# Optimization experiments

Measured on AMD Instinct MI355X. Metric: run time of the kernel, lower is better.

Reference implementation:

```python
import jax, jax.numpy as jnp
import numpy as np

B, S, D = 1, 8192, 4096
D_OUT = 4096
FP_FEATURES = 256
BITS = 4
MAXQ = float(2 ** BITS - 1)  # 15.0


def setup_inputs() -> dict:
    key = jax.random.key(0)
    kx, kw, kb, ks = jax.random.split(key, 4)
    x = jax.random.normal(kx, (B, S, D), dtype=jnp.float32)
    weight = jax.random.normal(kw, (D_OUT, D), dtype=jnp.float32) * 0.02
    bias = jax.random.normal(kb, (D_OUT,), dtype=jnp.float32) * 0.02
    # act_scales -> sorted indices; top FP_FEATURES stay in fp, rest quantized
    act_scales = jax.random.uniform(ks, (D,), dtype=jnp.float32)
    order = jnp.argsort(act_scales)
    q_idx = order[:-FP_FEATURES].astype(jnp.int64)
    fp_idx = order[-FP_FEATURES:].astype(jnp.int64)
    return {"x": x, "weight": weight, "bias": bias, "q_idx": q_idx, "fp_idx": fp_idx}


def reference(x, weight, bias, q_idx, fp_idx):
    # gather features to be quantized: [B, S, Dq]
    qf = x[:, :, q_idx]
    # per-token asymmetric quant params (find_params)
    xmin = jnp.minimum(qf.min(axis=-1), 0.0)
    xmax = jnp.maximum(qf.max(axis=-1), 0.0)
    both_zero = (xmin == 0.0) & (xmax == 0.0)
    xmin = jnp.where(both_zero, -1.0, xmin)
    xmax = jnp.where(both_zero, 1.0, xmax)
    scale = ((xmax - xmin) / MAXQ)[..., None]   # [B, S, 1]
    zero = jnp.round(-xmin[..., None] / scale)  # [B, S, 1]
    # asymmetric_quantize (fake quant)
    q = jnp.clip(jnp.round(qf / scale) + zero, 0.0, MAXQ)
    qf = scale * (q - zero)
    # scatter quantized + fp features back into a zeros_like buffer
    mixed = jnp.zeros_like(x)
    mixed = mixed.at[:, :, q_idx].set(qf)
    mixed = mixed.at[:, :, fp_idx].set(x[:, :, fp_idx])
    # wrapped Linear
    return mixed @ weight.T + bias
```

## Files before the change

### kernel.cpp

```cpp
#include <hip/hip_runtime.h>


typedef __attribute__((ext_vector_type(8))) short short8;
typedef __attribute__((ext_vector_type(4))) float f32x4;
typedef __attribute__((ext_vector_type(4))) int int4v;

#define S_ROWS 8192
#define D_IN   4096
#define D_OUTC 4096
#define MAXQF  15.0f

__device__ __forceinline__ unsigned short f2bf(float f) {
  unsigned int u = __float_as_uint(f);
  u += 0x7FFFu + ((u >> 16) & 1u);
  return (unsigned short)(u >> 16);
}

__global__ __launch_bounds__(256) void prep_kernel(const float* __restrict__ x,
                                                   const float* __restrict__ W,
                                                   const int* __restrict__ fp_idx,
                                                   signed char* __restrict__ actq,
                                                   signed char* __restrict__ wq,
                                                   short* __restrict__ xfp,
                                                   short* __restrict__ wfp,
                                                   float* __restrict__ as_,
                                                   float* __restrict__ ws_) {
  const int bid = blockIdx.x;
  const int t = threadIdx.x;
  __shared__ float s_r[4];

  if (bid >= S_ROWS) {
    const int row = bid - S_ROWS;
    const float* wr = W + (size_t)row * D_IN;
    float4 v[4];
    float mx = 0.0f;
#pragma unroll
    for (int i = 0; i < 4; ++i) {
      v[i] = ((const float4*)wr)[i * 256 + t];
      mx = fmaxf(mx, fmaxf(fmaxf(fabsf(v[i].x), fabsf(v[i].y)),
                           fmaxf(fabsf(v[i].z), fabsf(v[i].w))));
    }
#pragma unroll
    for (int d = 32; d > 0; d >>= 1) mx = fmaxf(mx, __shfl_xor(mx, d));
    if ((t & 63) == 0) s_r[t >> 6] = mx;
    __syncthreads();
    mx = fmaxf(fmaxf(s_r[0], s_r[1]), fmaxf(s_r[2], s_r[3]));
    const float wsr = (mx > 0.0f) ? (mx / 127.0f) : 1.0f;

    unsigned int* wrow = (unsigned int*)(wq + (size_t)row * D_IN);
#pragma unroll
    for (int i = 0; i < 4; ++i) {
      const float in[4] = { v[i].x, v[i].y, v[i].z, v[i].w };
      unsigned int pk = 0;
#pragma unroll
      for (int j = 0; j < 4; ++j) {
        int q = (int)fminf(fmaxf(rintf(in[j] / wsr), -127.0f), 127.0f);
        pk |= ((unsigned int)(unsigned char)(signed char)q) << (8 * j);
      }
      wrow[i * 256 + t] = pk;
    }
    wfp[(size_t)row * 256 + t] = (short)f2bf(wr[fp_idx[t]]);
    if (t == 0) ws_[row] = wsr;
    return;
  }

  __shared__ unsigned char fl[4096];
  ((int4*)fl)[t] = make_int4(0, 0, 0, 0);
  __syncthreads();
  fl[fp_idx[t]] = 1;
  __syncthreads();

  const int row = bid;
  const float* xr = x + (size_t)row * D_IN;

  float4 v[4];
  unsigned int fw[4];
  float mn = 0.0f, mx = 0.0f;
#pragma unroll
  for (int i = 0; i < 4; ++i) {
    const int idx = i * 256 + t;
    v[i] = ((const float4*)xr)[idx];
    fw[i] = ((const unsigned int*)fl)[idx];
    if (!(fw[i] & 0x000000FFu)) { mn = fminf(mn, v[i].x); mx = fmaxf(mx, v[i].x); }
    if (!(fw[i] & 0x0000FF00u)) { mn = fminf(mn, v[i].y); mx = fmaxf(mx, v[i].y); }
    if (!(fw[i] & 0x00FF0000u)) { mn = fminf(mn, v[i].z); mx = fmaxf(mx, v[i].z); }
    if (!(fw[i] & 0xFF000000u)) { mn = fminf(mn, v[i].w); mx = fmaxf(mx, v[i].w); }
  }
  __shared__ float s_mn[4];
#pragma unroll
  for (int d = 32; d > 0; d >>= 1) {
    mn = fminf(mn, __shfl_xor(mn, d));
    mx = fmaxf(mx, __shfl_xor(mx, d));
  }
  if ((t & 63) == 0) { s_mn[t >> 6] = mn; s_r[t >> 6] = mx; }
  __syncthreads();
  mn = fminf(fminf(s_mn[0], s_mn[1]), fminf(s_mn[2], s_mn[3]));
  mx = fmaxf(fmaxf(s_r[0], s_r[1]), fmaxf(s_r[2], s_r[3]));
  if (mn == 0.0f && mx == 0.0f) { mn = -1.0f; mx = 1.0f; }
  const float scale = (mx - mn) / MAXQF;
  const float zp = rintf(-mn / scale);
  const int zpi = (int)zp;

  unsigned int* arow = (unsigned int*)(actq + (size_t)row * D_IN);
#pragma unroll
  for (int i = 0; i < 4; ++i) {
    const int idx = i * 256 + t;
    const float in[4] = { v[i].x, v[i].y, v[i].z, v[i].w };
    const unsigned int f = fw[i];
    unsigned int pk = 0;
#pragma unroll
    for (int j = 0; j < 4; ++j) {
      int q = (int)fminf(fmaxf(rintf(in[j] / scale) + zp, 0.0f), MAXQF) - zpi;
      if ((f >> (8 * j)) & 0xFFu) q = 0;
      pk |= ((unsigned int)(unsigned char)(signed char)q) << (8 * j);
    }
    arow[idx] = pk;
  }
  xfp[(size_t)row * 256 + t] = (short)f2bf(xr[fp_idx[t]]);
  if (t == 0) as_[row] = scale;
}


__device__ __forceinline__ void gl2lds16(const void* g, const void* l) {
  __builtin_amdgcn_global_load_lds(
      (const __attribute__((address_space(1))) unsigned int*)g,
      (__attribute__((address_space(3))) unsigned int*)l, 16, 0, 0);
}

#define BARRIER()  asm volatile("s_barrier" ::: "memory")
#define LGKM0()    asm volatile("s_waitcnt lgkmcnt(0)" ::: "memory")

__global__ __launch_bounds__(512) void gemm_fp_kernel(const short* __restrict__ A,
                                                      const short* __restrict__ Bw,
                                                      const float* __restrict__ bias,
                                                      float* __restrict__ C) {
  __shared__ __align__(16) short lds[65536];
  const int tid = threadIdx.x;
  const int l   = tid & 63;
  const int w   = tid >> 6;
  const int wr  = w >> 2;
  const int wc  = w & 3;
  const int bid = blockIdx.x;
  const int swz = (bid & 7) * 64 + (bid >> 3);
  const int bm  = swz >> 4;
  const int bn  = swz & 15;

  const int c16  = ((l & 7) ^ (l >> 3)) * 8;
  const int rib0 = (w * 2 + 0) * 8 + (l >> 3);
  const int rib1 = (w * 2 + 1) * 8 + (l >> 3);
  const int d0   = (w * 2 + 0) * 512;
  const int d1   = (w * 2 + 1) * 512;
  const int LDK  = 256;

  const short* bA00 = A  + (size_t)(bm * 256 +   0 + rib0) * LDK + c16;
  const short* bA01 = A  + (size_t)(bm * 256 +   0 + rib1) * LDK + c16;
  const short* bA10 = A  + (size_t)(bm * 256 + 128 + rib0) * LDK + c16;
  const short* bA11 = A  + (size_t)(bm * 256 + 128 + rib1) * LDK + c16;
  const short* bB00 = Bw + (size_t)(bn * 256 +   0 + rib0) * LDK + c16;
  const short* bB01 = Bw + (size_t)(bn * 256 +   0 + rib1) * LDK + c16;
  const short* bB10 = Bw + (size_t)(bn * 256 + 128 + rib0) * LDK + c16;
  const short* bB11 = Bw + (size_t)(bn * 256 + 128 + rib1) * LDK + c16;

  gl2lds16(bA00, &lds[0 + d0]);          gl2lds16(bA01, &lds[0 + d1]);
  gl2lds16(bA10, &lds[8192 + d0]);       gl2lds16(bA11, &lds[8192 + d1]);
  gl2lds16(bB00, &lds[16384 + d0]);      gl2lds16(bB01, &lds[16384 + d1]);
  gl2lds16(bB10, &lds[24576 + d0]);      gl2lds16(bB11, &lds[24576 + d1]);
  gl2lds16(bA00 + 64, &lds[32768 + d0]); gl2lds16(bA01 + 64, &lds[32768 + d1]);
  gl2lds16(bA10 + 64, &lds[40960 + d0]); gl2lds16(bA11 + 64, &lds[40960 + d1]);
  asm volatile("s_waitcnt vmcnt(4)" ::: "memory");
  BARRIER();

  const short* pA00 = bA00 + 128; const short* pA01 = bA01 + 128;
  const short* pA10 = bA10 + 128; const short* pA11 = bA11 + 128;
  const short* pB00 = bB00 + 64;  const short* pB01 = bB01 + 64;
  const short* pB10 = bB10 + 64;  const short* pB11 = bB11 + 64;

  const int ch0  = ((l >> 4) ^ (l & 7)) * 8;
  const int aoff = wr * 8192 + (l & 15) * 64;
  const int boff = 16384 + (wc >> 1) * 8192 + (wc & 1) * 4096 + (l & 15) * 64;

  f32x4 acc[8][4] = {};
  int bo = 0;

  for (int t = 0; t < 4; ++t) {
    const int nxt = bo ^ 32768;
    short8 a0[4][2], a1[4][2], b[2][2];

#pragma unroll
    for (int m = 0; m < 4; ++m) {
      a0[m][0] = *(const short8*)&lds[bo + aoff + m * 1024 + ch0];
      a0[m][1] = *(const short8*)&lds[bo + aoff + m * 1024 + (ch0 ^ 32)];
    }
#pragma unroll
    for (int n = 0; n < 2; ++n) {
      b[n][0] = *(const short8*)&lds[bo + boff + n * 1024 + ch0];
      b[n][1] = *(const short8*)&lds[bo + boff + n * 1024 + (ch0 ^ 32)];
    }
    if (t < 3) { gl2lds16(pB00, &lds[nxt + 16384 + d0]);
                 gl2lds16(pB01, &lds[nxt + 16384 + d1]); }
    asm volatile("s_waitcnt lgkmcnt(8)" ::: "memory");
    BARRIER();
    LGKM0();
    __builtin_amdgcn_s_setprio(1);
#pragma unroll
    for (int m = 0; m < 4; ++m)
#pragma unroll
      for (int n = 0; n < 2; ++n) {
        acc[m][n] = __builtin_amdgcn_mfma_f32_16x16x32_bf16(a0[m][0], b[n][0], acc[m][n], 0, 0, 0);
        acc[m][n] = __builtin_amdgcn_mfma_f32_16x16x32_bf16(a0[m][1], b[n][1], acc[m][n], 0, 0, 0);
      }
    __builtin_amdgcn_s_setprio(0);
    BARRIER();

#pragma unroll
    for (int m = 0; m < 4; ++m) {
      a1[m][0] = *(const short8*)&lds[bo + aoff + (m + 4) * 1024 + ch0];
      a1[m][1] = *(const short8*)&lds[bo + aoff + (m + 4) * 1024 + (ch0 ^ 32)];
    }
    if (t < 3) { gl2lds16(pB10, &lds[nxt + 24576 + d0]);
                 gl2lds16(pB11, &lds[nxt + 24576 + d1]); }
    BARRIER();
    LGKM0();
    __builtin_amdgcn_s_setprio(1);
#pragma unroll
    for (int m = 0; m < 4; ++m)
#pragma unroll
      for (int n = 0; n < 2; ++n) {
        acc[m + 4][n] = __builtin_amdgcn_mfma_f32_16x16x32_bf16(a1[m][0], b[n][0], acc[m + 4][n], 0, 0, 0);
        acc[m + 4][n] = __builtin_amdgcn_mfma_f32_16x16x32_bf16(a1[m][1], b[n][1], acc[m + 4][n], 0, 0, 0);
      }
    __builtin_amdgcn_s_setprio(0);
    BARRIER();

#pragma unroll
    for (int n = 0; n < 2; ++n) {
      b[n][0] = *(const short8*)&lds[bo + boff + (n + 2) * 1024 + ch0];
      b[n][1] = *(const short8*)&lds[bo + boff + (n + 2) * 1024 + (ch0 ^ 32)];
    }
    if (t < 2) { gl2lds16(pA00, &lds[bo + 0 + d0]);
                 gl2lds16(pA01, &lds[bo + 0 + d1]); }
    BARRIER();
    LGKM0();
    __builtin_amdgcn_s_setprio(1);
#pragma unroll
    for (int m = 0; m < 4; ++m)
#pragma unroll
      for (int n = 0; n < 2; ++n) {
        acc[m + 4][n + 2] = __builtin_amdgcn_mfma_f32_16x16x32_bf16(a1[m][0], b[n][0], acc[m + 4][n + 2], 0, 0, 0);
        acc[m + 4][n + 2] = __builtin_amdgcn_mfma_f32_16x16x32_bf16(a1[m][1], b[n][1], acc[m + 4][n + 2], 0, 0, 0);
      }
    __builtin_amdgcn_s_setprio(0);
    BARRIER();

    if (t < 2) { gl2lds16(pA10, &lds[bo + 8192 + d0]);
                 gl2lds16(pA11, &lds[bo + 8192 + d1]); }
    BARRIER();
    __builtin_amdgcn_s_setprio(1);
#pragma unroll
    for (int m = 0; m < 4; ++m)
#pragma unroll
      for (int n = 0; n < 2; ++n) {
        acc[m][n + 2] = __builtin_amdgcn_mfma_f32_16x16x32_bf16(a0[m][0], b[n][0], acc[m][n + 2], 0, 0, 0);
        acc[m][n + 2] = __builtin_amdgcn_mfma_f32_16x16x32_bf16(a0[m][1], b[n][1], acc[m][n + 2], 0, 0, 0);
      }
    __builtin_amdgcn_s_setprio(0);
    if (t < 2) { asm volatile("s_waitcnt vmcnt(4)" ::: "memory"); }
    else       { asm volatile("s_waitcnt vmcnt(0)" ::: "memory"); }
    BARRIER();

    pA00 += 64; pA01 += 64; pA10 += 64; pA11 += 64;
    pB00 += 64; pB01 += 64; pB10 += 64; pB11 += 64;
    bo = nxt;
  }

  const int row0 = bm * 256 + wr * 128 + ((l >> 4) << 2);
  const int col0 = bn * 256 + wc * 64 + (l & 15);
#pragma unroll
  for (int m = 0; m < 8; ++m)
#pragma unroll
    for (int n = 0; n < 4; ++n) {
      const int col = col0 + n * 16;
      const float bv = bias[col];
#pragma unroll
      for (int r = 0; r < 4; ++r)
        C[(size_t)(row0 + m * 16 + r) * D_OUTC + col] = acc[m][n][r] + bv;
    }
}

__global__ __launch_bounds__(512) void gemm_i8_kernel(const signed char* __restrict__ A,
                                                      const signed char* __restrict__ Bw,
                                                      const float* __restrict__ as_,
                                                      const float* __restrict__ ws_,
                                                      float* __restrict__ C) {
  __shared__ __align__(16) signed char lds[131072];
  const int tid = threadIdx.x;
  const int l   = tid & 63;
  const int w   = tid >> 6;
  const int wr  = w >> 2;
  const int wc  = w & 3;
  const int bid = blockIdx.x;
  const int swz = (bid & 7) * 64 + (bid >> 3);
  const int bm  = swz >> 4;
  const int bn  = swz & 15;

  const int c16  = ((l & 7) ^ (l >> 3)) * 16;
  const int rib0 = (w * 2 + 0) * 8 + (l >> 3);
  const int rib1 = (w * 2 + 1) * 8 + (l >> 3);
  const int d0   = (w * 2 + 0) * 1024;
  const int d1   = (w * 2 + 1) * 1024;

  const signed char* bA00 = A  + (size_t)(bm * 256 +   0 + rib0) * D_IN + c16;
  const signed char* bA01 = A  + (size_t)(bm * 256 +   0 + rib1) * D_IN + c16;
  const signed char* bA10 = A  + (size_t)(bm * 256 + 128 + rib0) * D_IN + c16;
  const signed char* bA11 = A  + (size_t)(bm * 256 + 128 + rib1) * D_IN + c16;
  const signed char* bB00 = Bw + (size_t)(bn * 256 +   0 + rib0) * D_IN + c16;
  const signed char* bB01 = Bw + (size_t)(bn * 256 +   0 + rib1) * D_IN + c16;
  const signed char* bB10 = Bw + (size_t)(bn * 256 + 128 + rib0) * D_IN + c16;
  const signed char* bB11 = Bw + (size_t)(bn * 256 + 128 + rib1) * D_IN + c16;

  gl2lds16(bA00, &lds[0 + d0]);           gl2lds16(bA01, &lds[0 + d1]);
  gl2lds16(bA10, &lds[16384 + d0]);       gl2lds16(bA11, &lds[16384 + d1]);
  gl2lds16(bB00, &lds[32768 + d0]);       gl2lds16(bB01, &lds[32768 + d1]);
  gl2lds16(bB10, &lds[49152 + d0]);       gl2lds16(bB11, &lds[49152 + d1]);
  gl2lds16(bA00 + 128, &lds[65536 + d0]); gl2lds16(bA01 + 128, &lds[65536 + d1]);
  gl2lds16(bA10 + 128, &lds[81920 + d0]); gl2lds16(bA11 + 128, &lds[81920 + d1]);
  asm volatile("s_waitcnt vmcnt(4)" ::: "memory");
  BARRIER();

  const signed char* pA00 = bA00 + 256; const signed char* pA01 = bA01 + 256;
  const signed char* pA10 = bA10 + 256; const signed char* pA11 = bA11 + 256;
  const signed char* pB00 = bB00 + 128; const signed char* pB01 = bB01 + 128;
  const signed char* pB10 = bB10 + 128; const signed char* pB11 = bB11 + 128;

  const int ch0  = ((l >> 4) ^ (l & 7)) * 16;
  const int aoff = wr * 16384 + (l & 15) * 128;
  const int boff = 32768 + (wc >> 1) * 16384 + (wc & 1) * 8192 + (l & 15) * 128;

  int4v acc[8][4] = {};
  int bo = 0;

  for (int t = 0; t < 32; ++t) {
    const int nxt = bo ^ 65536;
    int4v a0[4][2], a1[4][2], b[2][2];

#pragma unroll
    for (int m = 0; m < 4; ++m) {
      a0[m][0] = *(const int4v*)&lds[bo + aoff + m * 2048 + ch0];
      a0[m][1] = *(const int4v*)&lds[bo + aoff + m * 2048 + (ch0 ^ 64)];
    }
#pragma unroll
    for (int n = 0; n < 2; ++n) {
      b[n][0] = *(const int4v*)&lds[bo + boff + n * 2048 + ch0];
      b[n][1] = *(const int4v*)&lds[bo + boff + n * 2048 + (ch0 ^ 64)];
    }
    if (t < 31) { gl2lds16(pB00, &lds[nxt + 32768 + d0]);
                  gl2lds16(pB01, &lds[nxt + 32768 + d1]); }
    asm volatile("s_waitcnt lgkmcnt(8)" ::: "memory");
    BARRIER();
    LGKM0();
    __builtin_amdgcn_s_setprio(1);
#pragma unroll
    for (int m = 0; m < 4; ++m)
#pragma unroll
      for (int n = 0; n < 2; ++n) {
        acc[m][n] = __builtin_amdgcn_mfma_i32_16x16x64_i8(a0[m][0], b[n][0], acc[m][n], 0, 0, 0);
        acc[m][n] = __builtin_amdgcn_mfma_i32_16x16x64_i8(a0[m][1], b[n][1], acc[m][n], 0, 0, 0);
      }
    __builtin_amdgcn_s_setprio(0);
    BARRIER();

#pragma unroll
    for (int m = 0; m < 4; ++m) {
      a1[m][0] = *(const int4v*)&lds[bo + aoff + (m + 4) * 2048 + ch0];
      a1[m][1] = *(const int4v*)&lds[bo + aoff + (m + 4) * 2048 + (ch0 ^ 64)];
    }
    if (t < 31) { gl2lds16(pB10, &lds[nxt + 49152 + d0]);
                  gl2lds16(pB11, &lds[nxt + 49152 + d1]); }
    BARRIER();
    LGKM0();
    __builtin_amdgcn_s_setprio(1);
#pragma unroll
    for (int m = 0; m < 4; ++m)
#pragma unroll
      for (int n = 0; n < 2; ++n) {
        acc[m + 4][n] = __builtin_amdgcn_mfma_i32_16x16x64_i8(a1[m][0], b[n][0], acc[m + 4][n], 0, 0, 0);
        acc[m + 4][n] = __builtin_amdgcn_mfma_i32_16x16x64_i8(a1[m][1], b[n][1], acc[m + 4][n], 0, 0, 0);
      }
    __builtin_amdgcn_s_setprio(0);
    BARRIER();

#pragma unroll
    for (int n = 0; n < 2; ++n) {
      b[n][0] = *(const int4v*)&lds[bo + boff + (n + 2) * 2048 + ch0];
      b[n][1] = *(const int4v*)&lds[bo + boff + (n + 2) * 2048 + (ch0 ^ 64)];
    }
    if (t < 30) { gl2lds16(pA00, &lds[bo + 0 + d0]);
                  gl2lds16(pA01, &lds[bo + 0 + d1]); }
    BARRIER();
    LGKM0();
    __builtin_amdgcn_s_setprio(1);
#pragma unroll
    for (int m = 0; m < 4; ++m)
#pragma unroll
      for (int n = 0; n < 2; ++n) {
        acc[m + 4][n + 2] = __builtin_amdgcn_mfma_i32_16x16x64_i8(a1[m][0], b[n][0], acc[m + 4][n + 2], 0, 0, 0);
        acc[m + 4][n + 2] = __builtin_amdgcn_mfma_i32_16x16x64_i8(a1[m][1], b[n][1], acc[m + 4][n + 2], 0, 0, 0);
      }
    __builtin_amdgcn_s_setprio(0);
    BARRIER();

    if (t < 30) { gl2lds16(pA10, &lds[bo + 16384 + d0]);
                  gl2lds16(pA11, &lds[bo + 16384 + d1]); }
    BARRIER();
    __builtin_amdgcn_s_setprio(1);
#pragma unroll
    for (int m = 0; m < 4; ++m)
#pragma unroll
      for (int n = 0; n < 2; ++n) {
        acc[m][n + 2] = __builtin_amdgcn_mfma_i32_16x16x64_i8(a0[m][0], b[n][0], acc[m][n + 2], 0, 0, 0);
        acc[m][n + 2] = __builtin_amdgcn_mfma_i32_16x16x64_i8(a0[m][1], b[n][1], acc[m][n + 2], 0, 0, 0);
      }
    __builtin_amdgcn_s_setprio(0);
    if (t < 30) { asm volatile("s_waitcnt vmcnt(4)" ::: "memory"); }
    else        { asm volatile("s_waitcnt vmcnt(0)" ::: "memory"); }
    BARRIER();

    pA00 += 128; pA01 += 128; pA10 += 128; pA11 += 128;
    pB00 += 128; pB01 += 128; pB10 += 128; pB11 += 128;
    bo = nxt;
  }

  const int row0 = bm * 256 + wr * 128 + ((l >> 4) << 2);
  const int col0 = bn * 256 + wc * 64 + (l & 15);
#pragma unroll
  for (int m = 0; m < 8; ++m)
#pragma unroll
    for (int n = 0; n < 4; ++n) {
      const int col = col0 + n * 16;
      const float wsv = ws_[col];
#pragma unroll
      for (int r = 0; r < 4; ++r) {
        const int row = row0 + m * 16 + r;
        const float s = as_[row] * wsv;
        float* cp = &C[(size_t)row * D_OUTC + col];
        *cp = *cp + s * (float)acc[m][n][r];
      }
    }
}

extern "C" void kernel_launch(void* const* d_in, const int* in_sizes, int n_in,
                              void* d_out, int out_size, void* d_ws, size_t ws_size,
                              hipStream_t stream) {
  const float* x    = (const float*)d_in[0];
  const float* W    = (const float*)d_in[1];
  const float* bias = (const float*)d_in[2];
  const int* fp_idx = (const int*)d_in[4];

  char* ws = (char*)d_ws;
  signed char* actq = (signed char*)ws;
  signed char* wq   = (signed char*)(ws + (32u << 20));
  short* xfp        = (short*)(ws + (48u << 20));
  short* wfp        = (short*)(ws + (52u << 20));
  float* as_        = (float*)(ws + (54u << 20));
  float* ws_        = (float*)(ws + (54u << 20) + (64u << 10));
  float* out = (float*)d_out;

  prep_kernel<<<S_ROWS + D_OUTC, 256, 0, stream>>>(x, W, fp_idx, actq, wq,
                                                   xfp, wfp, as_, ws_);
  gemm_fp_kernel<<<512, 512, 0, stream>>>(xfp, wfp, bias, out);
  gemm_i8_kernel<<<512, 512, 0, stream>>>(actq, wq, as_, ws_, out);
}
```

Measured before the change: 251.1 us.

## Fuse fp16 outlier GEMM into int8 GEMM kernel epilogue

Merges the separate bf16 outlier GEMM and int8 GEMM into one kernel. After the int8 main loop, accumulators are dequantized into float registers, then the bf16 K=256 GEMM accumulates on top, reusing the same LDS buffer, and bias is added on the single store. This removes one full write and read-modify-write pass over the fp32 output and one kernel launch, at the cost of a longer kernel and possible register pressure from the added launch bound.

```diff
diff --git a/kernel.cpp b/kernel.cpp
--- a/kernel.cpp
+++ b/kernel.cpp
@@ -130,168 +130,11 @@
 #define BARRIER()  asm volatile("s_barrier" ::: "memory")
 #define LGKM0()    asm volatile("s_waitcnt lgkmcnt(0)" ::: "memory")
 
-__global__ __launch_bounds__(512) void gemm_fp_kernel(const short* __restrict__ A,
-                                                      const short* __restrict__ Bw,
-                                                      const float* __restrict__ bias,
-                                                      float* __restrict__ C) {
-  __shared__ __align__(16) short lds[65536];
-  const int tid = threadIdx.x;
-  const int l   = tid & 63;
-  const int w   = tid >> 6;
-  const int wr  = w >> 2;
-  const int wc  = w & 3;
-  const int bid = blockIdx.x;
-  const int swz = (bid & 7) * 64 + (bid >> 3);
-  const int bm  = swz >> 4;
-  const int bn  = swz & 15;
-
-  const int c16  = ((l & 7) ^ (l >> 3)) * 8;
-  const int rib0 = (w * 2 + 0) * 8 + (l >> 3);
-  const int rib1 = (w * 2 + 1) * 8 + (l >> 3);
-  const int d0   = (w * 2 + 0) * 512;
-  const int d1   = (w * 2 + 1) * 512;
-  const int LDK  = 256;
-
-  const short* bA00 = A  + (size_t)(bm * 256 +   0 + rib0) * LDK + c16;
-  const short* bA01 = A  + (size_t)(bm * 256 +   0 + rib1) * LDK + c16;
-  const short* bA10 = A  + (size_t)(bm * 256 + 128 + rib0) * LDK + c16;
-  const short* bA11 = A  + (size_t)(bm * 256 + 128 + rib1) * LDK + c16;
-  const short* bB00 = Bw + (size_t)(bn * 256 +   0 + rib0) * LDK + c16;
-  const short* bB01 = Bw + (size_t)(bn * 256 +   0 + rib1) * LDK + c16;
-  const short* bB10 = Bw + (size_t)(bn * 256 + 128 + rib0) * LDK + c16;
-  const short* bB11 = Bw + (size_t)(bn * 256 + 128 + rib1) * LDK + c16;
-
-  gl2lds16(bA00, &lds[0 + d0]);          gl2lds16(bA01, &lds[0 + d1]);
-  gl2lds16(bA10, &lds[8192 + d0]);       gl2lds16(bA11, &lds[8192 + d1]);
-  gl2lds16(bB00, &lds[16384 + d0]);      gl2lds16(bB01, &lds[16384 + d1]);
-  gl2lds16(bB10, &lds[24576 + d0]);      gl2lds16(bB11, &lds[24576 + d1]);
-  gl2lds16(bA00 + 64, &lds[32768 + d0]); gl2lds16(bA01 + 64, &lds[32768 + d1]);
-  gl2lds16(bA10 + 64, &lds[40960 + d0]); gl2lds16(bA11 + 64, &lds[40960 + d1]);
-  asm volatile("s_waitcnt vmcnt(4)" ::: "memory");
-  BARRIER();
-
-  const short* pA00 = bA00 + 128; const short* pA01 = bA01 + 128;
-  const short* pA10 = bA10 + 128; const short* pA11 = bA11 + 128;
-  const short* pB00 = bB00 + 64;  const short* pB01 = bB01 + 64;
-  const short* pB10 = bB10 + 64;  const short* pB11 = bB11 + 64;
-
-  const int ch0  = ((l >> 4) ^ (l & 7)) * 8;
-  const int aoff = wr * 8192 + (l & 15) * 64;
-  const int boff = 16384 + (wc >> 1) * 8192 + (wc & 1) * 4096 + (l & 15) * 64;
-
-  f32x4 acc[8][4] = {};
-  int bo = 0;
-
-  for (int t = 0; t < 4; ++t) {
-    const int nxt = bo ^ 32768;
-    short8 a0[4][2], a1[4][2], b[2][2];
-
-#pragma unroll
-    for (int m = 0; m < 4; ++m) {
-      a0[m][0] = *(const short8*)&lds[bo + aoff + m * 1024 + ch0];
-      a0[m][1] = *(const short8*)&lds[bo + aoff + m * 1024 + (ch0 ^ 32)];
-    }
-#pragma unroll
-    for (int n = 0; n < 2; ++n) {
-      b[n][0] = *(const short8*)&lds[bo + boff + n * 1024 + ch0];
-      b[n][1] = *(const short8*)&lds[bo + boff + n * 1024 + (ch0 ^ 32)];
-    }
-    if (t < 3) { gl2lds16(pB00, &lds[nxt + 16384 + d0]);
-                 gl2lds16(pB01, &lds[nxt + 16384 + d1]); }
-    asm volatile("s_waitcnt lgkmcnt(8)" ::: "memory");
-    BARRIER();
-    LGKM0();
-    __builtin_amdgcn_s_setprio(1);
-#pragma unroll
-    for (int m = 0; m < 4; ++m)
-#pragma unroll
-      for (int n = 0; n < 2; ++n) {
-        acc[m][n] = __builtin_amdgcn_mfma_f32_16x16x32_bf16(a0[m][0], b[n][0], acc[m][n], 0, 0, 0);
-        acc[m][n] = __builtin_amdgcn_mfma_f32_16x16x32_bf16(a0[m][1], b[n][1], acc[m][n], 0, 0, 0);
-      }
-    __builtin_amdgcn_s_setprio(0);
-    BARRIER();
-
-#pragma unroll
-    for (int m = 0; m < 4; ++m) {
-      a1[m][0] = *(const short8*)&lds[bo + aoff + (m + 4) * 1024 + ch0];
-      a1[m][1] = *(const short8*)&lds[bo + aoff + (m + 4) * 1024 + (ch0 ^ 32)];
-    }
-    if (t < 3) { gl2lds16(pB10, &lds[nxt + 24576 + d0]);
-                 gl2lds16(pB11, &lds[nxt + 24576 + d1]); }
-    BARRIER();
-    LGKM0();
-    __builtin_amdgcn_s_setprio(1);
-#pragma unroll
-    for (int m = 0; m < 4; ++m)
-#pragma unroll
-      for (int n = 0; n < 2; ++n) {
-        acc[m + 4][n] = __builtin_amdgcn_mfma_f32_16x16x32_bf16(a1[m][0], b[n][0], acc[m + 4][n], 0, 0, 0);
-        acc[m + 4][n] = __builtin_amdgcn_mfma_f32_16x16x32_bf16(a1[m][1], b[n][1], acc[m + 4][n], 0, 0, 0);
-      }
-    __builtin_amdgcn_s_setprio(0);
-    BARRIER();
-
-#pragma unroll
-    for (int n = 0; n < 2; ++n) {
-      b[n][0] = *(const short8*)&lds[bo + boff + (n + 2) * 1024 + ch0];
-      b[n][1] = *(const short8*)&lds[bo + boff + (n + 2) * 1024 + (ch0 ^ 32)];
-    }
-    if (t < 2) { gl2lds16(pA00, &lds[bo + 0 + d0]);
-                 gl2lds16(pA01, &lds[bo + 0 + d1]); }
-    BARRIER();
-    LGKM0();
-    __builtin_amdgcn_s_setprio(1);
-#pragma unroll
-    for (int m = 0; m < 4; ++m)
-#pragma unroll
-      for (int n = 0; n < 2; ++n) {
-        acc[m + 4][n + 2] = __builtin_amdgcn_mfma_f32_16x16x32_bf16(a1[m][0], b[n][0], acc[m + 4][n + 2], 0, 0, 0);
-        acc[m + 4][n + 2] = __builtin_amdgcn_mfma_f32_16x16x32_bf16(a1[m][1], b[n][1], acc[m + 4][n + 2], 0, 0, 0);
-      }
-    __builtin_amdgcn_s_setprio(0);
-    BARRIER();
-
-    if (t < 2) { gl2lds16(pA10, &lds[bo + 8192 + d0]);
-                 gl2lds16(pA11, &lds[bo + 8192 + d1]); }
-    BARRIER();
-    __builtin_amdgcn_s_setprio(1);
-#pragma unroll
-    for (int m = 0; m < 4; ++m)
-#pragma unroll
-      for (int n = 0; n < 2; ++n) {
-        acc[m][n + 2] = __builtin_amdgcn_mfma_f32_16x16x32_bf16(a0[m][0], b[n][0], acc[m][n + 2], 0, 0, 0);
-        acc[m][n + 2] = __builtin_amdgcn_mfma_f32_16x16x32_bf16(a0[m][1], b[n][1], acc[m][n + 2], 0, 0, 0);
-      }
-    __builtin_amdgcn_s_setprio(0);
-    if (t < 2) { asm volatile("s_waitcnt vmcnt(4)" ::: "memory"); }
-    else       { asm volatile("s_waitcnt vmcnt(0)" ::: "memory"); }
-    BARRIER();
-
-    pA00 += 64; pA01 += 64; pA10 += 64; pA11 += 64;
-    pB00 += 64; pB01 += 64; pB10 += 64; pB11 += 64;
-    bo = nxt;
-  }
-
-  const int row0 = bm * 256 + wr * 128 + ((l >> 4) << 2);
-  const int col0 = bn * 256 + wc * 64 + (l & 15);
-#pragma unroll
-  for (int m = 0; m < 8; ++m)
-#pragma unroll
-    for (int n = 0; n < 4; ++n) {
-      const int col = col0 + n * 16;
-      const float bv = bias[col];
-#pragma unroll
-      for (int r = 0; r < 4; ++r)
-        C[(size_t)(row0 + m * 16 + r) * D_OUTC + col] = acc[m][n][r] + bv;
-    }
-}
-
-__global__ __launch_bounds__(512) void gemm_i8_kernel(const signed char* __restrict__ A,
-                                                      const signed char* __restrict__ Bw,
-                                                      const float* __restrict__ as_,
-                                                      const float* __restrict__ ws_,
-                                                      float* __restrict__ C) {
+__global__ __launch_bounds__(512, 2) void gemm_i8fp_kernel(
+    const signed char* __restrict__ A, const signed char* __restrict__ Bw,
+    const short* __restrict__ Afp, const short* __restrict__ Bfp,
+    const float* __restrict__ as_, const float* __restrict__ ws_,
+    const float* __restrict__ bias, float* __restrict__ C) {
   __shared__ __align__(16) signed char lds[131072];
   const int tid = threadIdx.x;
   const int l   = tid & 63;
@@ -432,19 +275,150 @@
 
   const int row0 = bm * 256 + wr * 128 + ((l >> 4) << 2);
   const int col0 = bn * 256 + wc * 64 + (l & 15);
+  f32x4 facc[8][4];
+#pragma unroll
+  for (int m = 0; m < 8; ++m)
+#pragma unroll
+    for (int n = 0; n < 4; ++n) {
+      const float wsv = ws_[col0 + n * 16];
+#pragma unroll
+      for (int r = 0; r < 4; ++r)
+        facc[m][n][r] = (float)acc[m][n][r] * (as_[row0 + m * 16 + r] * wsv);
+    }
+
+  short* sh = (short*)lds;
+  const int c16s = ((l & 7) ^ (l >> 3)) * 8;
+  const int LDK = 256;
+  const short* fA00 = Afp + (size_t)(bm * 256 +   0 + rib0) * LDK + c16s;
+  const short* fA01 = Afp + (size_t)(bm * 256 +   0 + rib1) * LDK + c16s;
+  const short* fA10 = Afp + (size_t)(bm * 256 + 128 + rib0) * LDK + c16s;
+  const short* fA11 = Afp + (size_t)(bm * 256 + 128 + rib1) * LDK + c16s;
+  const short* fB00 = Bfp + (size_t)(bn * 256 +   0 + rib0) * LDK + c16s;
+  const short* fB01 = Bfp + (size_t)(bn * 256 +   0 + rib1) * LDK + c16s;
+  const short* fB10 = Bfp + (size_t)(bn * 256 + 128 + rib0) * LDK + c16s;
+  const short* fB11 = Bfp + (size_t)(bn * 256 + 128 + rib1) * LDK + c16s;
+  const int ds0 = (w * 2 + 0) * 512;
+  const int ds1 = (w * 2 + 1) * 512;
+
+  gl2lds16(fA00, &sh[0 + ds0]);          gl2lds16(fA01, &sh[0 + ds1]);
+  gl2lds16(fA10, &sh[8192 + ds0]);       gl2lds16(fA11, &sh[8192 + ds1]);
+  gl2lds16(fB00, &sh[16384 + ds0]);      gl2lds16(fB01, &sh[16384 + ds1]);
+  gl2lds16(fB10, &sh[24576 + ds0]);      gl2lds16(fB11, &sh[24576 + ds1]);
+  gl2lds16(fA00 + 64, &sh[32768 + ds0]); gl2lds16(fA01 + 64, &sh[32768 + ds1]);
+  gl2lds16(fA10 + 64, &sh[40960 + ds0]); gl2lds16(fA11 + 64, &sh[40960 + ds1]);
+  asm volatile("s_waitcnt vmcnt(4)" ::: "memory");
+  BARRIER();
+
+  const short* qA00 = fA00 + 128; const short* qA01 = fA01 + 128;
+  const short* qA10 = fA10 + 128; const short* qA11 = fA11 + 128;
+  const short* qB00 = fB00 + 64;  const short* qB01 = fB01 + 64;
+  const short* qB10 = fB10 + 64;  const short* qB11 = fB11 + 64;
+
+  const int ch0s  = ((l >> 4) ^ (l & 7)) * 8;
+  const int aoffs = wr * 8192 + (l & 15) * 64;
+  const int boffs = 16384 + (wc >> 1) * 8192 + (wc & 1) * 4096 + (l & 15) * 64;
+
+  int sbo = 0;
+  for (int t = 0; t < 4; ++t) {
+    const int nxt = sbo ^ 32768;
+    short8 a0[4][2], a1[4][2], b[2][2];
+
+#pragma unroll
+    for (int m = 0; m < 4; ++m) {
+      a0[m][0] = *(const short8*)&sh[sbo + aoffs + m * 1024 + ch0s];
+      a0[m][1] = *(const short8*)&sh[sbo + aoffs + m * 1024 + (ch0s ^ 32)];
+    }
+#pragma unroll
+    for (int n = 0; n < 2; ++n) {
+      b[n][0] = *(const short8*)&sh[sbo + boffs + n * 1024 + ch0s];
+      b[n][1] = *(const short8*)&sh[sbo + boffs + n * 1024 + (ch0s ^ 32)];
+    }
+    if (t < 3) { gl2lds16(qB00, &sh[nxt + 16384 + ds0]);
+                 gl2lds16(qB01, &sh[nxt + 16384 + ds1]); }
+    asm volatile("s_waitcnt lgkmcnt(8)" ::: "memory");
+    BARRIER();
+    LGKM0();
+    __builtin_amdgcn_s_setprio(1);
+#pragma unroll
+    for (int m = 0; m < 4; ++m)
+#pragma unroll
+      for (int n = 0; n < 2; ++n) {
+        facc[m][n] = __builtin_amdgcn_mfma_f32_16x16x32_bf16(a0[m][0], b[n][0], facc[m][n], 0, 0, 0);
+        facc[m][n] = __builtin_amdgcn_mfma_f32_16x16x32_bf16(a0[m][1], b[n][1], facc[m][n], 0, 0, 0);
+      }
+    __builtin_amdgcn_s_setprio(0);
+    BARRIER();
+
+#pragma unroll
+    for (int m = 0; m < 4; ++m) {
+      a1[m][0] = *(const short8*)&sh[sbo + aoffs + (m + 4) * 1024 + ch0s];
+      a1[m][1] = *(const short8*)&sh[sbo + aoffs + (m + 4) * 1024 + (ch0s ^ 32)];
+    }
+    if (t < 3) { gl2lds16(qB10, &sh[nxt + 24576 + ds0]);
+                 gl2lds16(qB11, &sh[nxt + 24576 + ds1]); }
+    BARRIER();
+    LGKM0();
+    __builtin_amdgcn_s_setprio(1);
+#pragma unroll
+    for (int m = 0; m < 4; ++m)
+#pragma unroll
+      for (int n = 0; n < 2; ++n) {
+        facc[m + 4][n] = __builtin_amdgcn_mfma_f32_16x16x32_bf16(a1[m][0], b[n][0], facc[m + 4][n], 0, 0, 0);
+        facc[m + 4][n] = __builtin_amdgcn_mfma_f32_16x16x32_bf16(a1[m][1], b[n][1], facc[m + 4][n], 0, 0, 0);
+      }
+    __builtin_amdgcn_s_setprio(0);
+    BARRIER();
+
+#pragma unroll
+    for (int n = 0; n < 2; ++n) {
+      b[n][0] = *(const short8*)&sh[sbo + boffs + (n + 2) * 1024 + ch0s];
+      b[n][1] = *(const short8*)&sh[sbo + boffs + (n + 2) * 1024 + (ch0s ^ 32)];
+    }
+    if (t < 2) { gl2lds16(qA00, &sh[sbo + 0 + ds0]);
+                 gl2lds16(qA01, &sh[sbo + 0 + ds1]); }
+    BARRIER();
+    LGKM0();
+    __builtin_amdgcn_s_setprio(1);
+#pragma unroll
+    for (int m = 0; m < 4; ++m)
+#pragma unroll
+      for (int n = 0; n < 2; ++n) {
+        facc[m + 4][n + 2] = __builtin_amdgcn_mfma_f32_16x16x32_bf16(a1[m][0], b[n][0], facc[m + 4][n + 2], 0, 0, 0);
+        facc[m + 4][n + 2] = __builtin_amdgcn_mfma_f32_16x16x32_bf16(a1[m][1], b[n][1], facc[m + 4][n + 2], 0, 0, 0);
+      }
+    __builtin_amdgcn_s_setprio(0);
+    BARRIER();
+
+    if (t < 2) { gl2lds16(qA10, &sh[sbo + 8192 + ds0]);
+                 gl2lds16(qA11, &sh[sbo + 8192 + ds1]); }
+    BARRIER();
+    __builtin_amdgcn_s_setprio(1);
+#pragma unroll
+    for (int m = 0; m < 4; ++m)
+#pragma unroll
+      for (int n = 0; n < 2; ++n) {
+        facc[m][n + 2] = __builtin_amdgcn_mfma_f32_16x16x32_bf16(a0[m][0], b[n][0], facc[m][n + 2], 0, 0, 0);
+        facc[m][n + 2] = __builtin_amdgcn_mfma_f32_16x16x32_bf16(a0[m][1], b[n][1], facc[m][n + 2], 0, 0, 0);
+      }
+    __builtin_amdgcn_s_setprio(0);
+    if (t < 2) { asm volatile("s_waitcnt vmcnt(4)" ::: "memory"); }
+    else       { asm volatile("s_waitcnt vmcnt(0)" ::: "memory"); }
+    BARRIER();
+
+    qA00 += 64; qA01 += 64; qA10 += 64; qA11 += 64;
+    qB00 += 64; qB01 += 64; qB10 += 64; qB11 += 64;
+    sbo = nxt;
+  }
+
 #pragma unroll
   for (int m = 0; m < 8; ++m)
 #pragma unroll
     for (int n = 0; n < 4; ++n) {
       const int col = col0 + n * 16;
-      const float wsv = ws_[col];
-#pragma unroll
-      for (int r = 0; r < 4; ++r) {
-        const int row = row0 + m * 16 + r;
-        const float s = as_[row] * wsv;
-        float* cp = &C[(size_t)row * D_OUTC + col];
-        *cp = *cp + s * (float)acc[m][n][r];
-      }
+      const float bv = bias[col];
+#pragma unroll
+      for (int r = 0; r < 4; ++r)
+        C[(size_t)(row0 + m * 16 + r) * D_OUTC + col] = facc[m][n][r] + bv;
     }
 }
 
@@ -467,6 +441,6 @@
 
   prep_kernel<<<S_ROWS + D_OUTC, 256, 0, stream>>>(x, W, fp_idx, actq, wq,
                                                    xfp, wfp, as_, ws_);
-  gemm_fp_kernel<<<512, 512, 0, stream>>>(xfp, wfp, bias, out);
-  gemm_i8_kernel<<<512, 512, 0, stream>>>(actq, wq, as_, ws_, out);
+  gemm_i8fp_kernel<<<512, 512, 0, stream>>>(actq, wq, xfp, wfp, as_, ws_,
+                                            bias, out);
 }
```

New measurement: 232.8 us. -7.3%, faster.
